# Optimization experiments

Measured on AMD Instinct MI355X. Metric: run time of the kernel, lower is better.

Reference implementation:

```python
import jax, jax.numpy as jnp
import numpy as np

GROUPS = 1  # module-level groups arg


def adaptive_avg_pool(x, out_size):
    # Equal-tile average pool (exact match to torch AdaptiveAvgPool2d when H,W divisible by out_size)
    b, c, h, w = x.shape
    fh, fw = h // out_size, w // out_size
    return x.reshape(b, c, out_size, fh, out_size, fw).mean(axis=(3, 5))


def setup_inputs() -> dict:
    key = jax.random.key(0)
    k1, k2, k3, k4 = jax.random.split(key, 4)
    x = jax.random.normal(k1, (64, 128, 80, 80), jnp.float32)
    weight = jax.random.normal(k2, (128, 128, 3, 3), jnp.float32) * 0.05   # static conv weight [out, icg, k, k]
    w_att = jax.random.normal(k3, (16384, 1, 3, 3), jnp.float32) * 0.05    # conv_att weight (groups=icg=128)
    b_att = jax.random.normal(k4, (16384,), jnp.float32) * 0.05            # conv_att bias
    return {"x": x, "weight": weight, "w_att": w_att, "b_att": b_att}


def reference(x, weight, w_att, b_att):
    b, cin, h, w = x.shape
    out_ch, icg, k, _ = weight.shape  # icg = in_channels // groups
    pad = 1

    # attention branch: adaptive avg pool to (k+2), grouped 3x3 VALID conv -> [b, out*icg, k, k]
    avg = adaptive_avg_pool(x, k + 2)
    att = jax.lax.conv_general_dilated(avg, w_att, (1, 1), "VALID",
                                       feature_group_count=icg)
    att = jax.nn.sigmoid(att + b_att[None, :, None, None])
    att = att.reshape(b, out_ch, icg, k, k)

    # per-sample dynamic kernels
    dyn_w = weight[None] * att                    # [b, out, icg, k, k]

    # batch-grouped conv: fold batch into channels, groups = b * GROUPS
    xg = x.reshape(1, b * cin, h, w)
    wg = dyn_w.reshape(b * out_ch, icg, k, k)
    out = jax.lax.conv_general_dilated(xg, wg, (1, 1), [(pad, pad), (pad, pad)],
                                       feature_group_count=b * GROUPS)
    return out.reshape(b, out_ch, out.shape[-2], out.shape[-1])
```

## Files before the change

### kernel.cpp

```cpp
#include <hip/hip_runtime.h>

typedef __bf16 bf16;
typedef __bf16 bf16x8 __attribute__((ext_vector_type(8)));
typedef float f32x4 __attribute__((ext_vector_type(4)));

#define NB 64
#define NC 128
#define NOC 128
#define HW 80
#define HPAD 82

#define XT_BYTES  110166016L
#define W2_BYTES  18874368L
#define AVG_BYTES 819200L
#define WS_NEEDED (XT_BYTES + W2_BYTES + AVG_BYTES)

__global__ void pool_kernel(const float* __restrict__ x, float* __restrict__ avg) {
    int wave = (blockIdx.x * blockDim.x + threadIdx.x) >> 6;
    int lane = threadIdx.x & 63;
    int j = wave % 5; int t = wave / 5;
    int i = t % 5; t /= 5;
    int c = t & 127; int b = t >> 7;
    const float* src = x + (((long)(b * 128 + c) * 80) + i * 16) * 80 + j * 16;
    int ry = lane >> 2;
    int rx = (lane & 3) * 4;
    float4 v = *reinterpret_cast<const float4*>(src + ry * 80 + rx);
    float s = v.x + v.y + v.z + v.w;
    #pragma unroll
    for (int off = 32; off > 0; off >>= 1) s += __shfl_down(s, off, 64);
    if (lane == 0) avg[wave] = s * (1.0f / 256.0f);
}

__global__ void transpose_kernel(const float* __restrict__ x, bf16* __restrict__ xT) {
    __shared__ bf16 tile[64 * 68];
    int b = blockIdx.z, icb = blockIdx.y, pxb = blockIdx.x;
    int t = threadIdx.x;
    int pl = t & 63;
    int ig = t >> 6;
    const float* src = x + ((long)(b * 128 + icb * 64) * 6400) + pxb * 64;
    #pragma unroll
    for (int it = 0; it < 16; ++it) {
        int ic = ig * 16 + it;
        float v = src[(long)ic * 6400 + pl];
        tile[pl * 68 + ic] = (bf16)v;
    }
    __syncthreads();
    #pragma unroll
    for (int it = 0; it < 4; ++it) {
        int idx = it * 256 + t;
        int pxl = idx >> 4;
        int icq = idx & 15;
        int px = pxb * 64 + pxl;
        int Y = px / 80 + 1, X = px % 80 + 1;
        uint2 v = *reinterpret_cast<const uint2*>(&tile[pxl * 68 + icq * 4]);
        *reinterpret_cast<uint2*>(&xT[(((long)b * 82 + Y) * 82 + X) * 128 + icb * 64 + icq * 4]) = v;
    }
}

__global__ void att_kernel(const float* __restrict__ avg, const float* __restrict__ weight,
                           const float* __restrict__ w_att, const float* __restrict__ b_att,
                           bf16* __restrict__ W2) {
    __shared__ float sa[25];
    int b = blockIdx.x >> 7, och = blockIdx.x & 127;
    int ic = threadIdx.x;
    if (ic < 25) sa[ic] = avg[(long)blockIdx.x * 25 + ic];
    __syncthreads();
    int o = och * 128 + ic;
    float wa[9];
    #pragma unroll
    for (int j = 0; j < 9; ++j) wa[j] = w_att[(long)o * 9 + j];
    float bias = b_att[o];
    const float* wst = weight + (long)o * 9;
    #pragma unroll
    for (int kh = 0; kh < 3; ++kh) {
        #pragma unroll
        for (int kw = 0; kw < 3; ++kw) {
            float z = bias;
            #pragma unroll
            for (int di = 0; di < 3; ++di)
                #pragma unroll
                for (int dj = 0; dj < 3; ++dj)
                    z += sa[(kh + di) * 5 + (kw + dj)] * wa[di * 3 + dj];
            float s = 1.0f / (1.0f + __expf(-z));
            float dw = wst[kh * 3 + kw] * s;
            int p = kh * 3 + kw;
            W2[(((long)b * 9 + p) * 128 + och) * 128 + ic] = (bf16)dw;
        }
    }
}

__global__ __launch_bounds__(256, 2)
void conv_gemm(const bf16* __restrict__ xT, const bf16* __restrict__ W2,
               float* __restrict__ out) {
    __shared__ bf16 Xs[180 * 128];
    __shared__ bf16 Ws[128 * 64];
    int b = blockIdx.z;
    int px0 = blockIdx.x * 16;
    int py0 = blockIdx.y * 8;
    int t = threadIdx.x;
    int wave = t >> 6, lane = t & 63;
    int q = lane >> 4;
    int li = lane & 15;

    {
        const bf16* src = xT + (((long)b * 82 + py0) * 82 + px0) * 128;
        #pragma unroll
        for (int it = 0; it < 12; ++it) {
            int idx = it * 256 + t;
            if (idx < 2880) {
                int pf = idx >> 4, icb = idx & 15;
                int r = pf / 18, cx = pf - r * 18;
                uint4 v = *reinterpret_cast<const uint4*>(src + ((long)r * 82 + cx) * 128 + icb * 8);
                *reinterpret_cast<uint4*>(&Xs[pf * 128 + ((icb ^ (pf & 7)) * 8)]) = v;
            }
        }
    }

    f32x4 acc[4][4];
    #pragma unroll
    for (int i = 0; i < 4; ++i)
        #pragma unroll
        for (int j = 0; j < 4; ++j) acc[i][j] = (f32x4){0.f, 0.f, 0.f, 0.f};

    int ow = (wave >> 1) * 64;
    int nw = (wave & 1) * 64;

    for (int p = 0; p < 9; ++p) {
        int kh = p / 3, kw = p - kh * 3;
        for (int h = 0; h < 2; ++h) {
            __syncthreads();
            {
                const bf16* wsrc = W2 + ((long)b * 9 + p) * 128 * 128 + h * 64;
                #pragma unroll
                for (int it = 0; it < 4; ++it) {
                    int idx = it * 256 + t;
                    int och = idx >> 3, icb = idx & 7;
                    uint4 v = *reinterpret_cast<const uint4*>(wsrc + och * 128 + icb * 8);
                    *reinterpret_cast<uint4*>(&Ws[och * 64 + ((icb ^ (och & 7)) * 8)]) = v;
                }
            }
            __syncthreads();
            #pragma unroll
            for (int k2 = 0; k2 < 2; ++k2) {
                int ic0 = k2 * 32;
                bf16x8 af[4], bfr[4];
                #pragma unroll
                for (int mi = 0; mi < 4; ++mi) {
                    int och = ow + mi * 16 + li;
                    int icb = (ic0 >> 3) + q;
                    af[mi] = *reinterpret_cast<const bf16x8*>(&Ws[och * 64 + ((icb ^ (och & 7)) * 8)]);
                }
                #pragma unroll
                for (int ni = 0; ni < 4; ++ni) {
                    int n = nw + ni * 16 + li;
                    int oy = n >> 4, ox = n & 15;
                    int pf = (oy + kh) * 18 + ox + kw;
                    int icbx = h * 8 + (ic0 >> 3) + q;
                    bfr[ni] = *reinterpret_cast<const bf16x8*>(&Xs[pf * 128 + ((icbx ^ (pf & 7)) * 8)]);
                }
                #pragma unroll
                for (int mi = 0; mi < 4; ++mi)
                    #pragma unroll
                    for (int ni = 0; ni < 4; ++ni)
                        acc[mi][ni] = __builtin_amdgcn_mfma_f32_16x16x32_bf16(af[mi], bfr[ni], acc[mi][ni], 0, 0, 0);
            }
        }
    }

    #pragma unroll
    for (int mi = 0; mi < 4; ++mi) {
        #pragma unroll
        for (int ni = 0; ni < 4; ++ni) {
            int n = nw + ni * 16 + li;
            int oy = py0 + (n >> 4), ox = px0 + (n & 15);
            #pragma unroll
            for (int r = 0; r < 4; ++r) {
                int och = ow + mi * 16 + q * 4 + r;
                out[((long)(b * 128 + och) * 80 + oy) * 80 + ox] = acc[mi][ni][r];
            }
        }
    }
}

extern "C" void kernel_launch(void* const* d_in, const int* in_sizes, int n_in,
                              void* d_out, int out_size, void* d_ws, size_t ws_size,
                              hipStream_t stream) {
    const float* x      = (const float*)d_in[0];
    const float* weight = (const float*)d_in[1];
    const float* w_att  = (const float*)d_in[2];
    const float* b_att  = (const float*)d_in[3];
    float* out = (float*)d_out;

    if (ws_size < (size_t)WS_NEEDED) return;

    char* ws = (char*)d_ws;
    bf16* xT  = (bf16*)ws;
    bf16* W2  = (bf16*)(ws + XT_BYTES);
    float* avg = (float*)(ws + XT_BYTES + W2_BYTES);

    hipMemsetAsync(xT, 0, XT_BYTES, stream);

    pool_kernel<<<51200, 256, 0, stream>>>(x, avg);
    transpose_kernel<<<dim3(100, 2, 64), 256, 0, stream>>>(x, xT);
    att_kernel<<<8192, 128, 0, stream>>>(avg, weight, w_att, b_att, W2);
    conv_gemm<<<dim3(5, 10, 64), 256, 0, stream>>>(xT, W2, out);
}
```

Measured before the change: 567.2 us.

## Drop memset, zero halo in transpose, async LDS loads, direct weight reads

The full-workspace memset is replaced by an extra transpose block per sample that zeroes only the padding border. The transpose now handles all 128 channels per block using float4 loads and 16-byte stores. In the conv GEMM, the input tile is staged with global_load_lds direct-to-LDS loads, and the per-tap weight tile is no longer staged through shared memory. MFMA A fragments are read straight from global memory, which removes most barriers and lets occupancy be raised to 3 blocks. The cost is more global or L2 traffic for weights and some dependence on cache hits.

```diff
diff --git a/kernel.cpp b/kernel.cpp
--- a/kernel.cpp
+++ b/kernel.cpp
@@ -3,17 +3,17 @@
 typedef __bf16 bf16;
 typedef __bf16 bf16x8 __attribute__((ext_vector_type(8)));
 typedef float f32x4 __attribute__((ext_vector_type(4)));
-
-#define NB 64
-#define NC 128
-#define NOC 128
-#define HW 80
-#define HPAD 82
 
 #define XT_BYTES  110166016L
 #define W2_BYTES  18874368L
 #define AVG_BYTES 819200L
 #define WS_NEEDED (XT_BYTES + W2_BYTES + AVG_BYTES)
+
+__device__ __forceinline__ void gload_lds16(const bf16* g, bf16* l) {
+    __builtin_amdgcn_global_load_lds(
+        (__attribute__((address_space(1))) void*)g,
+        (__attribute__((address_space(3))) void*)l, 16, 0, 0);
+}
 
 __global__ void pool_kernel(const float* __restrict__ x, float* __restrict__ avg) {
     int wave = (blockIdx.x * blockDim.x + threadIdx.x) >> 6;
@@ -31,29 +31,48 @@
     if (lane == 0) avg[wave] = s * (1.0f / 256.0f);
 }
 
-__global__ void transpose_kernel(const float* __restrict__ x, bf16* __restrict__ xT) {
-    __shared__ bf16 tile[64 * 68];
-    int b = blockIdx.z, icb = blockIdx.y, pxb = blockIdx.x;
+#define TLDS 130
+__global__ __launch_bounds__(256)
+void transpose_kernel(const float* __restrict__ x, bf16* __restrict__ xT) {
+    __shared__ bf16 tile[64 * TLDS];
+    int b = blockIdx.y, pxb = blockIdx.x;
     int t = threadIdx.x;
-    int pl = t & 63;
-    int ig = t >> 6;
-    const float* src = x + ((long)(b * 128 + icb * 64) * 6400) + pxb * 64;
-    #pragma unroll
-    for (int it = 0; it < 16; ++it) {
-        int ic = ig * 16 + it;
-        float v = src[(long)ic * 6400 + pl];
-        tile[pl * 68 + ic] = (bf16)v;
+    bf16* xTb = xT + (long)b * 82 * 82 * 128;
+    if (pxb == 100) {
+        uint4 z = {0u, 0u, 0u, 0u};
+        for (int i = t; i < 5184; i += 256) {
+            int px = i >> 4, ch = i & 15;
+            int Y, X;
+            if (px < 82)       { Y = 0;            X = px;       }
+            else if (px < 164) { Y = 81;           X = px - 82;  }
+            else if (px < 244) { Y = px - 164 + 1; X = 0;        }
+            else               { Y = px - 244 + 1; X = 81;       }
+            *reinterpret_cast<uint4*>(&xTb[((long)Y * 82 + X) * 128 + ch * 8]) = z;
+        }
+        return;
+    }
+    int px0 = pxb * 64;
+    const float* xb = x + (long)b * 128 * 6400 + px0;
+    #pragma unroll
+    for (int it = 0; it < 8; ++it) {
+        int idx = it * 256 + t;
+        int c = idx >> 4, q = idx & 15;
+        float4 v = *reinterpret_cast<const float4*>(xb + (long)c * 6400 + q * 4);
+        tile[(q * 4 + 0) * TLDS + c] = (bf16)v.x;
+        tile[(q * 4 + 1) * TLDS + c] = (bf16)v.y;
+        tile[(q * 4 + 2) * TLDS + c] = (bf16)v.z;
+        tile[(q * 4 + 3) * TLDS + c] = (bf16)v.w;
     }
     __syncthreads();
     #pragma unroll
     for (int it = 0; it < 4; ++it) {
         int idx = it * 256 + t;
-        int pxl = idx >> 4;
-        int icq = idx & 15;
-        int px = pxb * 64 + pxl;
-        int Y = px / 80 + 1, X = px % 80 + 1;
-        uint2 v = *reinterpret_cast<const uint2*>(&tile[pxl * 68 + icq * 4]);
-        *reinterpret_cast<uint2*>(&xT[(((long)b * 82 + Y) * 82 + X) * 128 + icb * 64 + icq * 4]) = v;
+        int px = idx >> 4, co = idx & 15;
+        const unsigned* s = reinterpret_cast<const unsigned*>(&tile[px * TLDS + co * 8]);
+        uint4 v; v.x = s[0]; v.y = s[1]; v.z = s[2]; v.w = s[3];
+        int pg = px0 + px;
+        int Y = pg / 80 + 1, X = pg % 80 + 1;
+        *reinterpret_cast<uint4*>(&xTb[((long)Y * 82 + X) * 128 + co * 8]) = v;
     }
 }
 
@@ -89,30 +108,26 @@
     }
 }
 
-__global__ __launch_bounds__(256, 2)
+__global__ __launch_bounds__(256, 3)
 void conv_gemm(const bf16* __restrict__ xT, const bf16* __restrict__ W2,
                float* __restrict__ out) {
     __shared__ bf16 Xs[180 * 128];
-    __shared__ bf16 Ws[128 * 64];
     int b = blockIdx.z;
     int px0 = blockIdx.x * 16;
     int py0 = blockIdx.y * 8;
     int t = threadIdx.x;
     int wave = t >> 6, lane = t & 63;
-    int q = lane >> 4;
-    int li = lane & 15;
+    int q = lane >> 4, li = lane & 15;
 
     {
         const bf16* src = xT + (((long)b * 82 + py0) * 82 + px0) * 128;
-        #pragma unroll
-        for (int it = 0; it < 12; ++it) {
-            int idx = it * 256 + t;
-            if (idx < 2880) {
-                int pf = idx >> 4, icb = idx & 15;
-                int r = pf / 18, cx = pf - r * 18;
-                uint4 v = *reinterpret_cast<const uint4*>(src + ((long)r * 82 + cx) * 128 + icb * 8);
-                *reinterpret_cast<uint4*>(&Xs[pf * 128 + ((icb ^ (pf & 7)) * 8)]) = v;
-            }
+        for (int ch = wave; ch < 45; ch += 4) {
+            int pf = ch * 4 + (lane >> 4);
+            int slot = lane & 15;
+            int icb = slot ^ (pf & 7);
+            int r = pf / 18, cx = pf - r * 18;
+            gload_lds16(src + ((long)r * 82 + cx) * 128 + icb * 8,
+                        &Xs[ch * 512 + lane * 8]);
         }
     }
 
@@ -124,46 +139,32 @@
 
     int ow = (wave >> 1) * 64;
     int nw = (wave & 1) * 64;
-
+    int oyb = nw >> 4;
+
+    __syncthreads();
+
+    const bf16* wb = W2 + (long)b * 9 * 16384;
     for (int p = 0; p < 9; ++p) {
         int kh = p / 3, kw = p - kh * 3;
-        for (int h = 0; h < 2; ++h) {
-            __syncthreads();
-            {
-                const bf16* wsrc = W2 + ((long)b * 9 + p) * 128 * 128 + h * 64;
+        const bf16* wp = wb + p * 16384;
+        #pragma unroll
+        for (int k2 = 0; k2 < 4; ++k2) {
+            bf16x8 af[4], bfr[4];
+            #pragma unroll
+            for (int mi = 0; mi < 4; ++mi)
+                af[mi] = *reinterpret_cast<const bf16x8*>(
+                    wp + (ow + mi * 16 + li) * 128 + (k2 * 4 + q) * 8);
+            #pragma unroll
+            for (int ni = 0; ni < 4; ++ni) {
+                int pf = (oyb + ni + kh) * 18 + li + kw;
+                int slot = (k2 * 4 + q) ^ (pf & 7);
+                bfr[ni] = *reinterpret_cast<const bf16x8*>(&Xs[pf * 128 + slot * 8]);
+            }
+            #pragma unroll
+            for (int mi = 0; mi < 4; ++mi)
                 #pragma unroll
-                for (int it = 0; it < 4; ++it) {
-                    int idx = it * 256 + t;
-                    int och = idx >> 3, icb = idx & 7;
-                    uint4 v = *reinterpret_cast<const uint4*>(wsrc + och * 128 + icb * 8);
-                    *reinterpret_cast<uint4*>(&Ws[och * 64 + ((icb ^ (och & 7)) * 8)]) = v;
-                }
-            }
-            __syncthreads();
-            #pragma unroll
-            for (int k2 = 0; k2 < 2; ++k2) {
-                int ic0 = k2 * 32;
-                bf16x8 af[4], bfr[4];
-                #pragma unroll
-                for (int mi = 0; mi < 4; ++mi) {
-                    int och = ow + mi * 16 + li;
-                    int icb = (ic0 >> 3) + q;
-                    af[mi] = *reinterpret_cast<const bf16x8*>(&Ws[och * 64 + ((icb ^ (och & 7)) * 8)]);
-                }
-                #pragma unroll
-                for (int ni = 0; ni < 4; ++ni) {
-                    int n = nw + ni * 16 + li;
-                    int oy = n >> 4, ox = n & 15;
-                    int pf = (oy + kh) * 18 + ox + kw;
-                    int icbx = h * 8 + (ic0 >> 3) + q;
-                    bfr[ni] = *reinterpret_cast<const bf16x8*>(&Xs[pf * 128 + ((icbx ^ (pf & 7)) * 8)]);
-                }
-                #pragma unroll
-                for (int mi = 0; mi < 4; ++mi)
-                    #pragma unroll
-                    for (int ni = 0; ni < 4; ++ni)
-                        acc[mi][ni] = __builtin_amdgcn_mfma_f32_16x16x32_bf16(af[mi], bfr[ni], acc[mi][ni], 0, 0, 0);
-            }
+                for (int ni = 0; ni < 4; ++ni)
+                    acc[mi][ni] = __builtin_amdgcn_mfma_f32_16x16x32_bf16(af[mi], bfr[ni], acc[mi][ni], 0, 0, 0);
         }
     }
 
@@ -198,10 +199,8 @@
     bf16* W2  = (bf16*)(ws + XT_BYTES);
     float* avg = (float*)(ws + XT_BYTES + W2_BYTES);
 
-    hipMemsetAsync(xT, 0, XT_BYTES, stream);
-
     pool_kernel<<<51200, 256, 0, stream>>>(x, avg);
-    transpose_kernel<<<dim3(100, 2, 64), 256, 0, stream>>>(x, xT);
+    transpose_kernel<<<dim3(101, 64), 256, 0, stream>>>(x, xT);
     att_kernel<<<8192, 128, 0, stream>>>(avg, weight, w_att, b_att, W2);
     conv_gemm<<<dim3(5, 10, 64), 256, 0, stream>>>(xT, W2, out);
 }
```

After: 660.2 us. +16.4%, slower.
